# Kernel tuning notes

Measured on AMD Instinct MI355X. Metric: run time of the kernel, lower is better.

Reference implementation:

```python
import jax, jax.numpy as jnp
import numpy as np

SHAPES = [(64, 64), (32, 32), (16, 16), (8, 8)]  # (H,W) per level, strides 8..64 of a 512px image
D, NH, NLV, NP, NLAYERS, DFF = 256, 8, 4, 4, 6, 1024
HD = D // NH
B = 4


def setup_inputs() -> dict:
    key = jax.random.key(0)
    ks = jax.random.split(key, 32)
    inp = {}
    for l, (h, w) in enumerate(SHAPES):
        inp[f"src{l}"] = jax.random.normal(ks[l], (B, D, h, w), jnp.float32)
        inp[f"pos{l}"] = jax.random.normal(ks[4 + l], (B, D, h, w), jnp.float32)
    s = 0.02
    p = lambda k, shape: jax.random.normal(k, shape, jnp.float32) * s
    inp["level_embed"] = p(ks[8], (NLV, D))
    inp["W_so"] = p(ks[9], (NLAYERS, D, NH * NLV * NP * 2)); inp["b_so"] = p(ks[10], (NLAYERS, NH * NLV * NP * 2))
    inp["W_aw"] = p(ks[11], (NLAYERS, D, NH * NLV * NP)); inp["b_aw"] = p(ks[12], (NLAYERS, NH * NLV * NP))
    inp["W_v"] = p(ks[13], (NLAYERS, D, D)); inp["b_v"] = p(ks[14], (NLAYERS, D))
    inp["W_o"] = p(ks[15], (NLAYERS, D, D)); inp["b_o"] = p(ks[16], (NLAYERS, D))
    inp["g1"] = jnp.ones((NLAYERS, D)); inp["be1"] = jnp.zeros((NLAYERS, D))
    inp["W_f1"] = p(ks[17], (NLAYERS, D, DFF)); inp["b_f1"] = p(ks[18], (NLAYERS, DFF))
    inp["W_f2"] = p(ks[19], (NLAYERS, DFF, D)); inp["b_f2"] = p(ks[20], (NLAYERS, D))
    inp["g2"] = jnp.ones((NLAYERS, D)); inp["be2"] = jnp.zeros((NLAYERS, D))
    return inp


def _layernorm(x, g, b):
    m = x.mean(-1, keepdims=True)
    v = x.var(-1, keepdims=True)
    return (x - m) * jax.lax.rsqrt(v + 1e-5) * g + b


def _reference_points():
    refs = []
    for (H_, W_) in SHAPES:
        ry = (jnp.arange(H_, dtype=jnp.float32) + 0.5) / H_
        rx = (jnp.arange(W_, dtype=jnp.float32) + 0.5) / W_
        gy, gx = jnp.meshgrid(ry, rx, indexing="ij")
        refs.append(jnp.stack([gx.ravel(), gy.ravel()], -1))
    return jnp.concatenate(refs, 0)  # [S,2] (x,y); valid_ratios==1 so same per level


def _ms_deform_sample(value, loc, aw):
    # value [B,S,NH,HD]; loc [B,S,NH,NLV,NP,2] (x,y in [0,1]); aw [B,S,NH,NLV,NP]
    Bq, S = value.shape[:2]
    v = value.transpose(0, 2, 1, 3)  # [B,NH,S,HD]
    out = jnp.zeros((Bq, NH, S, HD), value.dtype)
    start = 0
    for l, (H_, W_) in enumerate(SHAPES):
        n = H_ * W_
        vl = v[:, :, start:start + n, :]  # [B,NH,H_*W_,HD]
        start += n
        # grid_sample(align_corners=False) semantics: pixel = loc*size - 0.5, zero padding
        x = loc[:, :, :, l, :, 0] * W_ - 0.5  # [B,S,NH,NP]
        y = loc[:, :, :, l, :, 1] * H_ - 0.5
        x0 = jnp.floor(x); y0 = jnp.floor(y)
        wx1 = x - x0; wy1 = y - y0
        acc = jnp.zeros((Bq, NH, S * NP, HD), value.dtype)
        corners = ((0, 0, (1 - wx1) * (1 - wy1)), (1, 0, wx1 * (1 - wy1)),
                   (0, 1, (1 - wx1) * wy1), (1, 1, wx1 * wy1))
        for dx, dy, wgt in corners:
            xi = x0 + dx; yi = y0 + dy
            valid = (xi >= 0) & (xi < W_) & (yi >= 0) & (yi < H_)
            idx = (jnp.clip(yi, 0, H_ - 1) * W_ + jnp.clip(xi, 0, W_ - 1)).astype(jnp.int32)
            idx = idx.transpose(0, 2, 1, 3).reshape(Bq, NH, S * NP)
            w = (wgt * valid).transpose(0, 2, 1, 3).reshape(Bq, NH, S * NP)
            g = jnp.take_along_axis(vl, idx[..., None], axis=2)  # [B,NH,S*NP,HD]
            acc = acc + w[..., None] * g
        acc = acc.reshape(Bq, NH, S, NP, HD)
        awl = aw[:, :, :, l, :].transpose(0, 2, 1, 3)  # [B,NH,S,NP]
        out = out + (acc * awl[..., None]).sum(3)
    return out.transpose(0, 2, 1, 3).reshape(Bq, S, D)


def reference(src0, src1, src2, src3, pos0, pos1, pos2, pos3, level_embed,
              W_so, b_so, W_aw, b_aw, W_v, b_v, W_o, b_o, g1, be1,
              W_f1, b_f1, W_f2, b_f2, g2, be2):
    srcs = [src0, src1, src2, src3]
    poss = [pos0, pos1, pos2, pos3]
    src_flat, pos_flat = [], []
    for l in range(NLV):
        src_flat.append(srcs[l].reshape(B, D, -1).transpose(0, 2, 1))
        pos_flat.append(poss[l].reshape(B, D, -1).transpose(0, 2, 1) + level_embed[l])
    src = jnp.concatenate(src_flat, 1)   # [B,S,D]
    pos = jnp.concatenate(pos_flat, 1)
    S = src.shape[1]
    ref = _reference_points()  # [S,2]
    normalizer = jnp.array([[w, h] for (h, w) in SHAPES], jnp.float32)  # [NLV,2] = (W,H)

    out = src
    for i in range(NLAYERS):
        q = out + pos
        off = (q @ W_so[i] + b_so[i]).reshape(B, S, NH, NLV, NP, 2)
        loc = ref[None, :, None, None, None, :] + off / normalizer[None, None, None, :, None, :]
        aw = jax.nn.softmax((q @ W_aw[i] + b_aw[i]).reshape(B, S, NH, NLV * NP), -1)
        aw = aw.reshape(B, S, NH, NLV, NP)
        val = (out @ W_v[i] + b_v[i]).reshape(B, S, NH, HD)
        att = _ms_deform_sample(val, loc, aw) @ W_o[i] + b_o[i]
        x = _layernorm(out + att, g1[i], be1[i])
        ffn = jax.nn.relu(x @ W_f1[i] + b_f1[i]) @ W_f2[i] + b_f2[i]
        out = _layernorm(x + ffn, g2[i], be2[i])

    spatial_shapes = jnp.array(SHAPES, jnp.int32)
    level_start_index = jnp.concatenate([jnp.zeros((1,), jnp.int32),
                                         jnp.cumsum(spatial_shapes.prod(1))[:-1]])
    return out, spatial_shapes, level_start_index
```

## Files before the change

kernel.cpp:

```cpp
#include <hip/hip_runtime.h>
#include <cstdint>

#define SSn 5440
#define TTn 21760
#define TD ((size_t)TTn*256)
#define NL 6

typedef short bf16x8 __attribute__((ext_vector_type(8)));
typedef float f32x4 __attribute__((ext_vector_type(4)));
typedef float f32x2 __attribute__((ext_vector_type(2)));
typedef unsigned short u16x4 __attribute__((ext_vector_type(4)));
typedef unsigned short ushort_t;

__device__ __forceinline__ ushort_t f2b(float f) {
  uint32_t x = __float_as_uint(f);
  uint32_t r = x + 0x7FFFu + ((x >> 16) & 1u);
  return (ushort_t)(r >> 16);
}
__device__ __forceinline__ float b2f(ushort_t u) {
  return __uint_as_float((uint32_t)u << 16);
}

__global__ __launch_bounds__(256) void prep_kernel(
    const float* __restrict__ s0, const float* __restrict__ p0,
    const float* __restrict__ s1, const float* __restrict__ p1,
    const float* __restrict__ s2, const float* __restrict__ p2,
    const float* __restrict__ s3, const float* __restrict__ p3,
    const float* __restrict__ lev,
    float* __restrict__ cur, ushort_t* __restrict__ cur_b,
    ushort_t* __restrict__ pos_b, ushort_t* __restrict__ q_b)
{
  __shared__ float ts[64][65];
  __shared__ float tp[64][65];
  int bx = blockIdx.x;
  int b = bx / 340, r = bx % 340;
  const float *sp, *pp; int l, HW, start, dt, ptile;
  if (r < 256)      { l=0; HW=4096; start=0;    sp=s0; pp=p0; dt=r>>6;       ptile=r&63; }
  else if (r < 320) { l=1; HW=1024; start=4096; sp=s1; pp=p1; dt=(r-256)>>4; ptile=(r-256)&15; }
  else if (r < 336) { l=2; HW=256;  start=5120; sp=s2; pp=p2; dt=(r-320)>>2; ptile=(r-320)&3; }
  else              { l=3; HW=64;   start=5376; sp=s3; pp=p3; dt=r-336;      ptile=0; }
  int d0 = dt * 64, pp0 = ptile * 64;
  int t = threadIdx.x;
  int rr = t >> 2, c4 = (t & 3) * 16;
  size_t ibase = ((size_t)b * 256 + d0 + rr) * HW + pp0;
  #pragma unroll
  for (int i = 0; i < 4; ++i) {
    f32x4 v = *(const f32x4*)(sp + ibase + c4 + i * 4);
    f32x4 w = *(const f32x4*)(pp + ibase + c4 + i * 4);
    #pragma unroll
    for (int j = 0; j < 4; ++j) { ts[c4 + i*4 + j][rr] = v[j]; tp[c4 + i*4 + j][rr] = w[j]; }
  }
  __syncthreads();
  int token = start + pp0 + rr;
  size_t obase = ((size_t)b * SSn + token) * 256 + d0;
  #pragma unroll
  for (int i = 0; i < 4; ++i) {
    f32x4 cv; u16x4 cb, pb, qb;
    #pragma unroll
    for (int j = 0; j < 4; ++j) {
      float c = ts[rr][c4 + i*4 + j];
      float p = tp[rr][c4 + i*4 + j] + lev[l * 256 + d0 + c4 + i*4 + j];
      cv[j] = c; cb[j] = f2b(c); pb[j] = f2b(p); qb[j] = f2b(c + p);
    }
    *(f32x4*)(cur + obase + c4 + i*4) = cv;
    *(u16x4*)(cur_b + obase + c4 + i*4) = cb;
    *(u16x4*)(pos_b + obase + c4 + i*4) = pb;
    *(u16x4*)(q_b + obase + c4 + i*4) = qb;
  }
}

__global__ __launch_bounds__(256) void wprep_kernel(
    const float* __restrict__ W_so, const float* __restrict__ W_aw,
    const float* __restrict__ W_v,  const float* __restrict__ W_o,
    const float* __restrict__ W_f1, const float* __restrict__ W_f2,
    ushort_t* __restrict__ wt)
{
  __shared__ float tile[64][65];
  int bx = blockIdx.x;
  int layer = bx / 184, r = bx % 184;
  int type, ti;
  if (r < 16)       { type = 0; ti = r; }
  else if (r < 24)  { type = 1; ti = r - 16; }
  else if (r < 40)  { type = 2; ti = r - 24; }
  else if (r < 56)  { type = 3; ti = r - 40; }
  else if (r < 120) { type = 4; ti = r - 56; }
  else              { type = 5; ti = r - 120; }
  const float* src;
  int K, N, dof;
  switch (type) {
    case 0: src = W_so + (size_t)layer * 65536;  K = 256;  N = 256;  dof = 0;      break;
    case 1: src = W_aw + (size_t)layer * 32768;  K = 256;  N = 128;  dof = 65536;  break;
    case 2: src = W_v  + (size_t)layer * 65536;  K = 256;  N = 256;  dof = 98304;  break;
    case 3: src = W_o  + (size_t)layer * 65536;  K = 256;  N = 256;  dof = 163840; break;
    case 4: src = W_f1 + (size_t)layer * 262144; K = 256;  N = 1024; dof = 229376; break;
    default:src = W_f2 + (size_t)layer * 262144; K = 1024; N = 256;  dof = 491520; break;
  }
  int Kt = K >> 6;
  int k0 = (ti % Kt) * 64, n0 = (ti / Kt) * 64;
  ushort_t* dst = wt + (size_t)layer * 753664 + dof;
  int t = threadIdx.x;
  int rr = t >> 2, c4 = (t & 3) * 16;
  #pragma unroll
  for (int i = 0; i < 4; ++i) {
    f32x4 v = *(const f32x4*)(src + (size_t)(k0 + rr) * N + n0 + c4 + i * 4);
    tile[c4 + i*4 + 0][rr] = v[0];
    tile[c4 + i*4 + 1][rr] = v[1];
    tile[c4 + i*4 + 2][rr] = v[2];
    tile[c4 + i*4 + 3][rr] = v[3];
  }
  __syncthreads();
  #pragma unroll
  for (int i = 0; i < 4; ++i) {
    u16x4 o;
    #pragma unroll
    for (int j = 0; j < 4; ++j) o[j] = f2b(tile[rr][c4 + i*4 + j]);
    *(u16x4*)(dst + (size_t)(n0 + rr) * K + k0 + c4 + i * 4) = o;
  }
}

__global__ void bias_fuse(const float* __restrict__ bso,
                          const float* __restrict__ baw,
                          float* __restrict__ bsa)
{
  int l = blockIdx.x, t = threadIdx.x;
  bsa[l * 384 + t] = (t < 256) ? bso[l * 256 + t] : baw[l * 128 + t - 256];
}

__device__ __forceinline__ void gemm_body(
    ushort_t* As, ushort_t* Bs,
    const ushort_t* __restrict__ A, const ushort_t* __restrict__ Bt,
    const float* __restrict__ bias, ushort_t* __restrict__ Cb,
    int N, int n0, int m0, int K, int relu)
{
  int t = threadIdx.x;
  int l = t & 63, w = t >> 6;
  int wr = w >> 1, wc = w & 1;
  int lq = l >> 4, l15 = l & 15, r7 = l & 7;
  f32x4 acc[4][4] = {};

  for (int k0 = 0; k0 < K; k0 += 64) {
    #pragma unroll
    for (int i = 0; i < 4; ++i) {
      int c = i * 256 + t;
      int row = c >> 3;
      int sc = (c & 7) ^ (row & 7);
      __builtin_amdgcn_global_load_lds(
          (const uint32_t*)(A + (size_t)(m0 + row) * K + k0 + sc * 8),
          (uint32_t*)((char*)As + c * 16), 16, 0, 0);
      __builtin_amdgcn_global_load_lds(
          (const uint32_t*)(Bt + (size_t)(n0 + row) * K + k0 + sc * 8),
          (uint32_t*)((char*)Bs + c * 16), 16, 0, 0);
    }
    __syncthreads();
    #pragma unroll
    for (int ks = 0; ks < 2; ++ks) {
      bf16x8 af[4], bfr[4];
      int chs = ((ks << 2) + lq) ^ r7;
      #pragma unroll
      for (int mt = 0; mt < 4; ++mt)
        af[mt] = *(const bf16x8*)((const char*)As +
                   (wr * 64 + mt * 16 + l15) * 128 + (chs << 4));
      #pragma unroll
      for (int nt = 0; nt < 4; ++nt)
        bfr[nt] = *(const bf16x8*)((const char*)Bs +
                   (wc * 64 + nt * 16 + l15) * 128 + (chs << 4));
      #pragma unroll
      for (int mt = 0; mt < 4; ++mt)
        #pragma unroll
        for (int nt = 0; nt < 4; ++nt)
          acc[mt][nt] = __builtin_amdgcn_mfma_f32_16x16x32_bf16(
              af[mt], bfr[nt], acc[mt][nt], 0, 0, 0);
    }
    __syncthreads();
  }

  int crow0 = m0 + wr * 64;
  int ccol0 = n0 + wc * 64;
  #pragma unroll
  for (int mt = 0; mt < 4; ++mt) {
    #pragma unroll
    for (int nt = 0; nt < 4; ++nt) {
      int col = ccol0 + nt * 16 + l15;
      float bv = bias[col];
      #pragma unroll
      for (int r = 0; r < 4; ++r) {
        int rowg = crow0 + mt * 16 + lq * 4 + r;
        float v = acc[mt][nt][r] + bv;
        if (relu) v = fmaxf(v, 0.f);
        Cb[(size_t)rowg * N + col] = f2b(v);
      }
    }
  }
}

__global__ __launch_bounds__(256) void gemm_mfma(
    const ushort_t* __restrict__ A, const ushort_t* __restrict__ Bt,
    const float* __restrict__ bias, ushort_t* __restrict__ Cb,
    int N, int K, int relu)
{
  __shared__ alignas(16) ushort_t As[8192];
  __shared__ alignas(16) ushort_t Bs[8192];
  gemm_body(As, Bs, A, Bt, bias, Cb, N, blockIdx.y * 128, blockIdx.x * 128, K, relu);
}

__global__ __launch_bounds__(256) void gemm_dual(
    const ushort_t* __restrict__ A0, const ushort_t* __restrict__ Bt0,
    const float* __restrict__ bias0, ushort_t* __restrict__ C0,
    const ushort_t* __restrict__ A1, const ushort_t* __restrict__ Bt1,
    const float* __restrict__ bias1, ushort_t* __restrict__ C1,
    int K)
{
  __shared__ alignas(16) ushort_t As[8192];
  __shared__ alignas(16) ushort_t Bs[8192];
  int gy = blockIdx.y;
  if (gy < 3)
    gemm_body(As, Bs, A0, Bt0, bias0, C0, 384, gy * 128, blockIdx.x * 128, K, 0);
  else
    gemm_body(As, Bs, A1, Bt1, bias1, C1, 256, (gy - 3) * 128, blockIdx.x * 128, K, 0);
}

__global__ __launch_bounds__(256) void gemm_ln(
    const ushort_t* __restrict__ A, const ushort_t* __restrict__ Bt,
    const float* __restrict__ bias, const float* __restrict__ res,
    const float* __restrict__ g, const float* __restrict__ be,
    float* __restrict__ Of, ushort_t* __restrict__ Ob,
    ushort_t* __restrict__ Oq, const ushort_t* __restrict__ posb,
    int K)
{
  __shared__ alignas(16) ushort_t As[32 * 64];
  __shared__ alignas(16) ushort_t Bs[256 * 64];
  __shared__ float psum[32][4];
  __shared__ float psum2[32][4];
  __shared__ float2 mstd[32];
  int t = threadIdx.x;
  int l = t & 63, w = t >> 6;
  int m0 = blockIdx.x * 32;
  int lq = l >> 4, l15 = l & 15, r7 = l & 7;
  f32x4 acc[2][4] = {};

  for (int k0 = 0; k0 < K; k0 += 64) {
    {
      int c = t;
      int row = c >> 3;
      int sc = (c & 7) ^ (row & 7);
      __builtin_amdgcn_global_load_lds(
          (const uint32_t*)(A + (size_t)(m0 + row) * K + k0 + sc * 8),
          (uint32_t*)((char*)As + c * 16), 16, 0, 0);
    }
    #pragma unroll
    for (int i = 0; i < 8; ++i) {
      int c = i * 256 + t;
      int row = c >> 3;
      int sc = (c & 7) ^ (row & 7);
      __builtin_amdgcn_global_load_lds(
          (const uint32_t*)(Bt + (size_t)row * K + k0 + sc * 8),
          (uint32_t*)((char*)Bs + c * 16), 16, 0, 0);
    }
    __syncthreads();
    #pragma unroll
    for (int ks = 0; ks < 2; ++ks) {
      bf16x8 af[2], bfr[4];
      int chs = ((ks << 2) + lq) ^ r7;
      #pragma unroll
      for (int mt = 0; mt < 2; ++mt)
        af[mt] = *(const bf16x8*)((const char*)As +
                   (mt * 16 + l15) * 128 + (chs << 4));
      #pragma unroll
      for (int nt = 0; nt < 4; ++nt)
        bfr[nt] = *(const bf16x8*)((const char*)Bs +
                   (w * 64 + nt * 16 + l15) * 128 + (chs << 4));
      #pragma unroll
      for (int mt = 0; mt < 2; ++mt)
        #pragma unroll
        for (int nt = 0; nt < 4; ++nt)
          acc[mt][nt] = __builtin_amdgcn_mfma_f32_16x16x32_bf16(
              af[mt], bfr[nt], acc[mt][nt], 0, 0, 0);
    }
    __syncthreads();
  }

  float gv[4], bev[4], biasv[4];
  #pragma unroll
  for (int nt = 0; nt < 4; ++nt) {
    int col = w * 64 + nt * 16 + l15;
    gv[nt] = g[col]; bev[nt] = be[col]; biasv[nt] = bias[col];
  }
  #pragma unroll
  for (int mt = 0; mt < 2; ++mt) {
    #pragma unroll
    for (int r = 0; r < 4; ++r) {
      int rowg = m0 + mt * 16 + lq * 4 + r;
      #pragma unroll
      for (int nt = 0; nt < 4; ++nt) {
        int col = w * 64 + nt * 16 + l15;
        acc[mt][nt][r] += biasv[nt] + res[(size_t)rowg * 256 + col];
      }
    }
  }
  #pragma unroll
  for (int mt = 0; mt < 2; ++mt) {
    #pragma unroll
    for (int r = 0; r < 4; ++r) {
      float s = 0.f, s2 = 0.f;
      #pragma unroll
      for (int nt = 0; nt < 4; ++nt) {
        float v = acc[mt][nt][r];
        s += v; s2 += v * v;
      }
      #pragma unroll
      for (int off = 1; off < 16; off <<= 1) {
        s  += __shfl_xor(s, off);
        s2 += __shfl_xor(s2, off);
      }
      if (l15 == 0) {
        int rloc = mt * 16 + lq * 4 + r;
        psum[rloc][w] = s;
        psum2[rloc][w] = s2;
      }
    }
  }
  __syncthreads();
  if (t < 32) {
    f32x4 a = *(const f32x4*)psum[t];
    f32x4 b = *(const f32x4*)psum2[t];
    float s = a[0] + a[1] + a[2] + a[3];
    float s2 = b[0] + b[1] + b[2] + b[3];
    float mean = s * (1.f / 256.f);
    float var = s2 * (1.f / 256.f) - mean * mean;
    mstd[t] = make_float2(mean, rsqrtf(var + 1e-5f));
  }
  __syncthreads();
  #pragma unroll
  for (int mt = 0; mt < 2; ++mt) {
    #pragma unroll
    for (int r = 0; r < 4; ++r) {
      int rloc = mt * 16 + lq * 4 + r;
      int rowg = m0 + rloc;
      float2 ms = mstd[rloc];
      #pragma unroll
      for (int nt = 0; nt < 4; ++nt) {
        int col = w * 64 + nt * 16 + l15;
        float y = (acc[mt][nt][r] - ms.x) * ms.y * gv[nt] + bev[nt];
        size_t o = (size_t)rowg * 256 + col;
        Of[o] = y;
        Ob[o] = f2b(y);
        if (Oq) Oq[o] = f2b(y + b2f(posb[o]));
      }
    }
  }
}

__global__ __launch_bounds__(256) void sample_kernel(
    const ushort_t* __restrict__ val, const ushort_t* __restrict__ sa,
    ushort_t* __restrict__ att)
{
  __shared__ ushort4 sIdxU[8][136];
  __shared__ float4  sW4[8][136];
  int tid = threadIdx.x;
  int t0 = blockIdx.x * 8;

  #pragma unroll
  for (int it = 0; it < 4; ++it) {
    int idx = it * 256 + tid;
    int tl = idx >> 7;
    int pt = idx & 127;
    int t = t0 + tl;
    int b = t / SSn, s = t % SSn;
    int lvl = (pt >> 2) & 3;
    int st, Wt;
    if (s < 4096)      { st = 0;    Wt = 64; }
    else if (s < 5120) { st = 4096; Wt = 32; }
    else if (s < 5376) { st = 5120; Wt = 16; }
    else               { st = 5376; Wt = 8;  }
    int p = s - st;
    int iy = p / Wt, ix = p % Wt;
    float refx = (ix + 0.5f) / Wt;
    float refy = (iy + 0.5f) / Wt;

    float logit = b2f(sa[(size_t)t * 384 + 256 + pt]);
    float m = logit;
    #pragma unroll
    for (int off = 1; off < 16; off <<= 1) m = fmaxf(m, __shfl_xor(m, off));
    float e = __expf(logit - m);
    float sum = e;
    #pragma unroll
    for (int off = 1; off < 16; off <<= 1) sum += __shfl_xor(sum, off);
    float wa = e / sum;

    const int LWt[4] = {64, 32, 16, 8};
    const int LST[4] = {0, 4096, 5120, 5376};
    int Wl = LWt[lvl], Hl = Wl, stl = LST[lvl];

    float ox = b2f(sa[(size_t)t * 384 + pt * 2]);
    float oy = b2f(sa[(size_t)t * 384 + pt * 2 + 1]);
    float x = refx * Wl + ox - 0.5f;
    float y = refy * Hl + oy - 0.5f;
    float x0f = floorf(x), y0f = floorf(y);
    int x0 = (int)x0f, y0 = (int)y0f;
    float wx1 = x - x0f, wy1 = y - y0f;
    int vbase = b * SSn + stl;
    ushort4 idxu; float4 w4;
    float* wp = (float*)&w4;
    unsigned short* ip = (unsigned short*)&idxu;
    #pragma unroll
    for (int c = 0; c < 4; ++c) {
      int dx = c & 1, dy = c >> 1;
      int xi = x0 + dx, yi = y0 + dy;
      float wgt = (dx ? wx1 : 1.f - wx1) * (dy ? wy1 : 1.f - wy1);
      bool valid = (xi >= 0) & (xi < Wl) & (yi >= 0) & (yi < Hl);
      int xc = min(max(xi, 0), Wl - 1), yc = min(max(yi, 0), Hl - 1);
      ip[c] = (unsigned short)(vbase + yc * Wl + xc);
      wp[c] = valid ? wgt * wa : 0.f;
    }
    int pi = pt + (pt >> 4);
    sIdxU[tl][pi] = idxu;
    sW4[tl][pi] = w4;
  }
  __syncthreads();

  int tl = tid >> 5, v = tid & 31;
  int t = t0 + tl;
  int h = v >> 2, j = v & 3;
  int c0 = h * 32 + j * 8;
  f32x2 ac[4] = {};
  #pragma unroll
  for (int k = 0; k < 16; ++k) {
    int pi = h * 17 + k;
    ushort4 idxu = sIdxU[tl][pi];
    float4 w4 = sW4[tl][pi];
    const unsigned short* ip = (const unsigned short*)&idxu;
    const float* wp = (const float*)&w4;
    #pragma unroll
    for (int c = 0; c < 4; ++c) {
      uint4 uv = *(const uint4*)(val + ((size_t)ip[c] << 8) + c0);
      float wv = wp[c];
      f32x2 w2 = {wv, wv};
      f32x2 p0 = {__uint_as_float(uv.x << 16), __uint_as_float(uv.x & 0xFFFF0000u)};
      f32x2 p1 = {__uint_as_float(uv.y << 16), __uint_as_float(uv.y & 0xFFFF0000u)};
      f32x2 p2 = {__uint_as_float(uv.z << 16), __uint_as_float(uv.z & 0xFFFF0000u)};
      f32x2 p3 = {__uint_as_float(uv.w << 16), __uint_as_float(uv.w & 0xFFFF0000u)};
      ac[0] += w2 * p0;
      ac[1] += w2 * p1;
      ac[2] += w2 * p2;
      ac[3] += w2 * p3;
    }
  }
  uint4 pk;
  pk.x = (uint32_t)f2b(ac[0][0]) | ((uint32_t)f2b(ac[0][1]) << 16);
  pk.y = (uint32_t)f2b(ac[1][0]) | ((uint32_t)f2b(ac[1][1]) << 16);
  pk.z = (uint32_t)f2b(ac[2][0]) | ((uint32_t)f2b(ac[2][1]) << 16);
  pk.w = (uint32_t)f2b(ac[3][0]) | ((uint32_t)f2b(ac[3][1]) << 16);
  *(uint4*)(att + (size_t)t * 256 + c0) = pk;
}

__global__ void tail_kernel(float* __restrict__ o) {
  const float v[12] = {64.f, 64.f, 32.f, 32.f, 16.f, 16.f, 8.f, 8.f,
                       0.f, 4096.f, 5120.f, 5376.f};
  int i = threadIdx.x;
  if (i < 12) o[i] = v[i];
}

extern "C" void kernel_launch(void* const* d_in, const int* in_sizes, int n_in,
                              void* d_out, int out_size, void* d_ws, size_t ws_size,
                              hipStream_t stream)
{
  const float* s0  = (const float*)d_in[0];
  const float* p0  = (const float*)d_in[1];
  const float* s1  = (const float*)d_in[2];
  const float* p1  = (const float*)d_in[3];
  const float* s2  = (const float*)d_in[4];
  const float* p2  = (const float*)d_in[5];
  const float* s3  = (const float*)d_in[6];
  const float* p3  = (const float*)d_in[7];
  const float* lev = (const float*)d_in[8];
  const float* W_so = (const float*)d_in[9];
  const float* b_so = (const float*)d_in[10];
  const float* W_aw = (const float*)d_in[11];
  const float* b_aw = (const float*)d_in[12];
  const float* W_v  = (const float*)d_in[13];
  const float* b_v  = (const float*)d_in[14];
  const float* W_o  = (const float*)d_in[15];
  const float* b_o  = (const float*)d_in[16];
  const float* g1   = (const float*)d_in[17];
  const float* be1  = (const float*)d_in[18];
  const float* W_f1 = (const float*)d_in[19];
  const float* b_f1 = (const float*)d_in[20];
  const float* W_f2 = (const float*)d_in[21];
  const float* b_f2 = (const float*)d_in[22];
  const float* g2   = (const float*)d_in[23];
  const float* be2  = (const float*)d_in[24];

  float* out = (float*)d_out;
  float* ws  = (float*)d_ws;

  ushort_t* pos_b = (ushort_t*)ws;
  float*    x_f   = ws + TD / 2;
  ushort_t* q_b   = (ushort_t*)(ws + TD / 2 + TD);
  ushort_t* cur_b = (ushort_t*)(ws + 2 * TD);
  ushort_t* x_b   = (ushort_t*)(ws + 2 * TD + TD / 2);
  ushort_t* sa_b  = (ushort_t*)(ws + 3 * TD);
  ushort_t* val_b = (ushort_t*)(ws + 3 * TD + 3 * (TD / 4));
  ushort_t* h_b   = (ushort_t*)(ws + 3 * TD);
  ushort_t* wt    = (ushort_t*)(ws + 5 * TD);
  float*    bsa   = ws + 5 * TD + 2260992;

  const size_t LW = 753664;

  wprep_kernel<<<1104, 256, 0, stream>>>(W_so, W_aw, W_v, W_o, W_f1, W_f2, wt);
  bias_fuse<<<NL, 384, 0, stream>>>(b_so, b_aw, bsa);
  prep_kernel<<<1360, 256, 0, stream>>>(s0, p0, s1, p1, s2, p2, s3, p3, lev,
                                        out, cur_b, pos_b, q_b);

  for (int i = 0; i < NL; ++i) {
    ushort_t* wl = wt + (size_t)i * LW;
    const float* bv  = b_v  + (size_t)i * 256;
    const float* bo  = b_o  + (size_t)i * 256;
    const float* bf1 = b_f1 + (size_t)i * 1024;
    const float* bf2 = b_f2 + (size_t)i * 256;

    gemm_dual<<<dim3(170, 5), 256, 0, stream>>>(q_b, wl + 0, bsa + i * 384, sa_b,
                                                cur_b, wl + 98304, bv, val_b, 256);
    sample_kernel<<<TTn / 8, 256, 0, stream>>>(val_b, sa_b, q_b);
    gemm_ln<<<680, 256, 0, stream>>>(q_b, wl + 163840, bo, out,
                                     g1 + i * 256, be1 + i * 256,
                                     x_f, x_b, nullptr, nullptr, 256);
    gemm_mfma<<<dim3(170, 8), 256, 0, stream>>>(x_b, wl + 229376, bf1,
                                                h_b, 1024, 256, 1);
    gemm_ln<<<680, 256, 0, stream>>>(h_b, wl + 491520, bf2, x_f,
                                     g2 + i * 256, be2 + i * 256,
                                     out, cur_b, q_b, pos_b, 1024);
  }

  tail_kernel<<<1, 16, 0, stream>>>(out + TD);
}
```

Measured before the change: 789.0 us.

## Pack sampling records into 16-byte LDS entries and swizzle block order

Corner indices and bilinear weights are packed into a single 16-byte record per sample point, with weights stored as bf16 instead of fp32. This halves shared memory per block and needs one LDS read per point instead of two. Block indices are remapped so consecutive blocks are spread across the token range, likely to balance level/batch locality across XCDs, and launch bounds now request higher occupancy. Storing weights in bf16 loses some precision in the sampling weights.

```diff
diff --git a/kernel.cpp b/kernel.cpp
--- a/kernel.cpp
+++ b/kernel.cpp
@@ -350,14 +350,14 @@
   }
 }
 
-__global__ __launch_bounds__(256) void sample_kernel(
+__global__ __launch_bounds__(256, 8) void sample_kernel(
     const ushort_t* __restrict__ val, const ushort_t* __restrict__ sa,
     ushort_t* __restrict__ att)
 {
-  __shared__ ushort4 sIdxU[8][136];
-  __shared__ float4  sW4[8][136];
+  __shared__ uint4 rec[8][136];
   int tid = threadIdx.x;
-  int t0 = blockIdx.x * 8;
+  int bid = blockIdx.x;
+  int t0 = ((bid & 7) * 340 + (bid >> 3)) * 8;
 
   #pragma unroll
   for (int it = 0; it < 4; ++it) {
@@ -399,9 +399,7 @@
     int x0 = (int)x0f, y0 = (int)y0f;
     float wx1 = x - x0f, wy1 = y - y0f;
     int vbase = b * SSn + stl;
-    ushort4 idxu; float4 w4;
-    float* wp = (float*)&w4;
-    unsigned short* ip = (unsigned short*)&idxu;
+    uint32_t ipk[4]; uint32_t wpk[4];
     #pragma unroll
     for (int c = 0; c < 4; ++c) {
       int dx = c & 1, dy = c >> 1;
@@ -409,12 +407,15 @@
       float wgt = (dx ? wx1 : 1.f - wx1) * (dy ? wy1 : 1.f - wy1);
       bool valid = (xi >= 0) & (xi < Wl) & (yi >= 0) & (yi < Hl);
       int xc = min(max(xi, 0), Wl - 1), yc = min(max(yi, 0), Hl - 1);
-      ip[c] = (unsigned short)(vbase + yc * Wl + xc);
-      wp[c] = valid ? wgt * wa : 0.f;
-    }
-    int pi = pt + (pt >> 4);
-    sIdxU[tl][pi] = idxu;
-    sW4[tl][pi] = w4;
+      ipk[c] = (uint32_t)(vbase + yc * Wl + xc);
+      wpk[c] = valid ? (uint32_t)f2b(wgt * wa) : 0u;
+    }
+    uint4 r;
+    r.x = ipk[0] | (ipk[1] << 16);
+    r.y = ipk[2] | (ipk[3] << 16);
+    r.z = wpk[0] | (wpk[1] << 16);
+    r.w = wpk[2] | (wpk[3] << 16);
+    rec[tl][pt + (pt >> 4)] = r;
   }
   __syncthreads();
 
@@ -425,16 +426,16 @@
   f32x2 ac[4] = {};
   #pragma unroll
   for (int k = 0; k < 16; ++k) {
-    int pi = h * 17 + k;
-    ushort4 idxu = sIdxU[tl][pi];
-    float4 w4 = sW4[tl][pi];
-    const unsigned short* ip = (const unsigned short*)&idxu;
-    const float* wp = (const float*)&w4;
+    uint4 r = rec[tl][h * 17 + k];
+    uint32_t id[4] = { r.x & 0xFFFFu, r.x >> 16, r.y & 0xFFFFu, r.y >> 16 };
+    float wv[4] = { __uint_as_float(r.z << 16),
+                    __uint_as_float(r.z & 0xFFFF0000u),
+                    __uint_as_float(r.w << 16),
+                    __uint_as_float(r.w & 0xFFFF0000u) };
     #pragma unroll
     for (int c = 0; c < 4; ++c) {
-      uint4 uv = *(const uint4*)(val + ((size_t)ip[c] << 8) + c0);
-      float wv = wp[c];
-      f32x2 w2 = {wv, wv};
+      uint4 uv = *(const uint4*)(val + ((size_t)id[c] << 8) + c0);
+      f32x2 w2 = {wv[c], wv[c]};
       f32x2 p0 = {__uint_as_float(uv.x << 16), __uint_as_float(uv.x & 0xFFFF0000u)};
       f32x2 p1 = {__uint_as_float(uv.y << 16), __uint_as_float(uv.y & 0xFFFF0000u)};
       f32x2 p2 = {__uint_as_float(uv.z << 16), __uint_as_float(uv.z & 0xFFFF0000u)};
```

Measured after the change: 790.0 us. About the same (+0.1%).
